# Performance work log

Measured on AMD Instinct MI355X. Metric: run time of the kernel, lower is better.

## Reference

```python
import jax, jax.numpy as jnp
import numpy as np

EPS = 1e-4
SILU_GAIN = 1.0 / 0.596  # magnitude-preserving SiLU gain
SCALES = (4, 4, 8)       # prod == A_DIM == 128
T = 0.3                  # residual lerp weight


def mp_silu(x):
    return jax.nn.silu(x) * SILU_GAIN


def pixel_norm(x):
    # normalize over channel dim (axis=1) to unit RMS
    return x * jax.lax.rsqrt(jnp.mean(jnp.square(x), axis=1, keepdims=True) + EPS)


def norm_w(w):
    # magnitude-preserving conv: per-output-filter L2-normalized weight
    n = jnp.sqrt(jnp.sum(jnp.square(w), axis=tuple(range(1, w.ndim)), keepdims=True) + 1e-8)
    return w / n


def mp_add(a, b, t=T):
    return (a * (1.0 - t) + b * t) / np.sqrt((1.0 - t) ** 2 + t ** 2)


def conv2d(x, w, groups=1, padding=((0, 0), (0, 0))):
    return jax.lax.conv_general_dilated(
        x, w, (1, 1), padding,
        dimension_numbers=('NCHW', 'OIHW', 'NCHW'), feature_group_count=groups)


def conv1d(x, w, groups=1, padding=((0, 0),)):
    return jax.lax.conv_general_dilated(
        x, w, (1,), padding,
        dimension_numbers=('NCH', 'OIH', 'NCH'), feature_group_count=groups)


def avgpool_freq(x, s):
    B, C, F, L = x.shape
    return jnp.mean(x.reshape(B, C, F // s, s, L), axis=3)


def min_gru(h, w):
    # minGRU: z_t = sigmoid(Wz h_t), c_t = Wc h_t, s_t = (1-z_t) s_{t-1} + z_t c_t
    z, c = jnp.split(conv1d(h, norm_w(w)), 2, axis=1)
    z = jax.nn.sigmoid(z)
    a, b = 1.0 - z, z * c  # linear recurrence s_t = a_t s_{t-1} + b_t

    def comb(x, y):
        a1, b1 = x
        a2, b2 = y
        return a2 * a1, a2 * b1 + b2

    _, out = jax.lax.associative_scan(comb, (a, b), axis=-1)
    return out


def conv_block(x, w1, wd, w2, wdn, s):
    # x: [B, d, F, L]
    x = pixel_norm(x)
    r = mp_silu(x)
    r = conv2d(r, norm_w(w1))                                            # d -> h, 1x1
    r = conv2d(r, norm_w(wd), groups=wd.shape[0], padding=((2, 2), (1, 1)))  # depthwise 5x3
    r = mp_silu(r)
    r = conv2d(r, norm_w(w2))                                            # h -> d, 1x1
    h = mp_add(x, r)
    return conv2d(avgpool_freq(h, s), norm_w(wdn))                       # d -> 2d, freq /s


def seq_block(x, hg_w, dw_w, gru_w, out_w):
    # x: [B, d, L]
    x = pixel_norm(x)
    h, g = jnp.split(conv1d(x, norm_w(hg_w)), 2, axis=1)  # each [B, H, L]
    h = mp_silu(h)
    h = conv1d(h, norm_w(dw_w), groups=dw_w.shape[0], padding=((1, 1),))  # depthwise k=3
    h = mp_silu(h)
    h = min_gru(h, gru_w)
    h = h * mp_silu(g)
    return mp_add(x, conv1d(h, norm_w(out_w)))


def setup_inputs() -> dict:
    key = jax.random.key(0)
    ks = jax.random.split(key, 18)
    rn = lambda k, s: jax.random.normal(k, s, dtype=jnp.float32)
    B, L, A = 2, 2048, 128
    return {
        'audio': rn(ks[0], (B, A, L)),
        'proj_w': rn(ks[1], (64, 1, 1, 1)) * 0.5,
        'proj_b': jnp.zeros((64,), jnp.float32),
        'c0_w1': rn(ks[2], (128, 64, 1, 1)),
        'c0_wd': rn(ks[3], (128, 1, 5, 3)),
        'c0_w2': rn(ks[4], (64, 128, 1, 1)),
        'c0_dn': rn(ks[5], (128, 64, 1, 1)),
        'c1_w1': rn(ks[6], (256, 128, 1, 1)),
        'c1_wd': rn(ks[7], (256, 1, 5, 3)),
        'c1_w2': rn(ks[8], (128, 256, 1, 1)),
        'c1_dn': rn(ks[9], (256, 128, 1, 1)),
        'c2_w1': rn(ks[10], (512, 256, 1, 1)),
        'c2_wd': rn(ks[11], (512, 1, 5, 3)),
        'c2_w2': rn(ks[12], (256, 512, 1, 1)),
        'c2_dn': rn(ks[13], (512, 256, 1, 1)),
        'hg_w': rn(ks[14], (4, 2048, 512, 1)),
        'dw_w': rn(ks[15], (4, 1024, 1, 3)),
        'gru_w': rn(ks[16], (4, 2048, 1024, 1)),
        'out_w': rn(ks[17], (4, 512, 1024, 1)),
    }


def reference(audio, proj_w, proj_b,
              c0_w1, c0_wd, c0_w2, c0_dn,
              c1_w1, c1_wd, c1_w2, c1_dn,
              c2_w1, c2_wd, c2_w2, c2_dn,
              hg_w, dw_w, gru_w, out_w):
    h = audio[:, None]  # [B, 1, A_DIM, L]
    h = conv2d(h, proj_w) + proj_b[None, :, None, None]
    blocks = ((c0_w1, c0_wd, c0_w2, c0_dn),
              (c1_w1, c1_wd, c1_w2, c1_dn),
              (c2_w1, c2_wd, c2_w2, c2_dn))
    for (w1, wd, w2, dn), s in zip(blocks, SCALES):
        h = conv_block(h, w1, wd, w2, dn, s)
    h = h[:, :, 0, :]  # freq dim reduced to 1 -> [B, dim, L]
    for i in range(hg_w.shape[0]):
        h = seq_block(h, hg_w[i], dw_w[i], gru_w[i], out_w[i])
    return mp_silu(h)
```

## Files before the change

kernel.cpp:

```cpp
#include <hip/hip_runtime.h>
#include <math.h>

#define GAIN 1.6778523489932886f
#define MPS  1.3130643285972254f

typedef __attribute__((ext_vector_type(8))) short short8;
typedef __attribute__((ext_vector_type(4))) short short4v;
typedef __attribute__((ext_vector_type(4))) float float4v;

__device__ __forceinline__ float silu_g(float x){
  float s = 1.0f/(1.0f + __expf(-x));
  return x*s*GAIN;
}
__device__ __forceinline__ short f2bf(float f){
  unsigned u = __builtin_bit_cast(unsigned, f);
  u += 0x7fffu + ((u >> 16) & 1u);
  return (short)(u >> 16);
}
__device__ __forceinline__ float bf2f(unsigned short h){
  return __builtin_bit_cast(float, ((unsigned)h) << 16);
}

typedef __attribute__((address_space(3))) unsigned int as3_uint;
typedef const __attribute__((address_space(1))) unsigned int as1_cuint;
__device__ __forceinline__ void gload16(const unsigned short* gsrc, unsigned short* ldst){
  __builtin_amdgcn_global_load_lds((as1_cuint*)gsrc, (as3_uint*)ldst, 16, 0, 0);
}

struct NcEnt { const float* w; int O, K, dstOff; };
struct NcArgs { NcEnt e[16]; };

__global__ __launch_bounds__(64) void normcast_kernel(NcArgs na, unsigned short* __restrict__ wbf){
  int row = blockIdx.x;
  int base = 0; int i;
  for (i = 0; i < 16; i++){
    if (row < base + na.e[i].O) break;
    base += na.e[i].O;
  }
  if (i >= 16) return;
  int r = row - base; int K = na.e[i].K;
  const float* w = na.e[i].w + (long)r*K;
  unsigned short* dst = wbf + na.e[i].dstOff + (long)r*K;
  int tid = threadIdx.x;
  float s = 0.f;
  const bool v4 = ((K & 3) == 0);
  if (v4){
    for (int k = tid*4; k < K; k += 256){
      float4v v = *(const float4v*)&w[k];
      s += v[0]*v[0] + v[1]*v[1] + v[2]*v[2] + v[3]*v[3];
    }
  } else {
    for (int k = tid; k < K; k += 64){ float v = w[k]; s += v*v; }
  }
  for (int off = 32; off; off >>= 1) s += __shfl_down(s, off);
  float inv = rsqrtf(__shfl(s, 0) + 1e-8f);
  if (v4){
    for (int k = tid*4; k < K; k += 256){
      float4v v = *(const float4v*)&w[k];
      short4v o = { f2bf(v[0]*inv), f2bf(v[1]*inv), f2bf(v[2]*inv), f2bf(v[3]*inv) };
      *(short4v*)&dst[k] = o;
    }
  } else {
    for (int k = tid; k < K; k += 64) dst[k] = (unsigned short)f2bf(w[k]*inv);
  }
}

__global__ __launch_bounds__(64) void projstats_kernel(const float* __restrict__ pw, const float* __restrict__ pb,
                                                       float* __restrict__ S){
  int t = threadIdx.x;
  float p = pw[t], q = pb[t];
  float s1 = p*p, s2 = p*q, s3 = q*q;
  for (int off = 32; off; off >>= 1){
    s1 += __shfl_down(s1, off); s2 += __shfl_down(s2, off); s3 += __shfl_down(s3, off);
  }
  if (t == 0){ S[0] = s1; S[1] = s2; S[2] = s3; }
}

__global__ __launch_bounds__(256) void invn_audio_kernel(const float* __restrict__ audio, const float* __restrict__ S,
                                                         float* __restrict__ invn){
  long i = blockIdx.x*256 + threadIdx.x;
  if (i >= (2L*128*2048)/4) return;
  long e = i*4;
  float S1 = S[0], S2 = S[1], S3 = S[2];
  float4v a = *(const float4v*)&audio[e];
  float4v o;
  #pragma unroll
  for (int j = 0; j < 4; j++) o[j] = rsqrtf((a[j]*a[j]*S1 + 2.f*a[j]*S2 + S3)/64.f + 1e-4f);
  *(float4v*)&invn[e] = o;
}

template<int G, bool BF>
__global__ __launch_bounds__(256) void invn_reduce_kernel(const void* __restrict__ Xv, float* __restrict__ invn,
                                                          int C, int F){
  constexpr int L = 256/G;
  int t = threadIdx.x; int cs = t / L; int li = t % L;
  long pos = (long)blockIdx.x*L + li;
  int bf = (int)(pos >> 11); int l = (int)(pos & 2047);
  int b = bf / F; int f = bf - b*F;
  long base = ((long)b*C*F + f)*2048 + l;
  long stride = (long)F*2048;
  float s = 0.f;
  if (BF){
    const unsigned short* X = (const unsigned short*)Xv;
    for (int c = cs; c < C; c += G){ float v = bf2f(X[base + (long)c*stride]); s += v*v; }
  } else {
    const float* X = (const float*)Xv;
    for (int c = cs; c < C; c += G){ float v = X[base + (long)c*stride]; s += v*v; }
  }
  __shared__ float red[256];
  red[t] = s; __syncthreads();
  #pragma unroll
  for (int off = G/2; off > 0; off >>= 1){
    if (cs < off) red[t] += red[t + off*L];
    __syncthreads();
  }
  if (cs == 0) invn[pos] = rsqrtf(red[li]/(float)C + 1e-4f);
}

template<bool SILU, bool BF>
__global__ __launch_bounds__(256) void applynorm_kernel(const void* __restrict__ Xv, const float* __restrict__ invn,
                                                        unsigned short* __restrict__ XB, int C, int F, long total4){
  long i = blockIdx.x*256 + threadIdx.x;
  if (i >= total4) return;
  long e = i*4;
  int l = (int)(e & 2047); long r = e >> 11;
  int f = (int)(r % F); long bc = r / F; int b = (int)(bc / C);
  float4v x;
  if (BF){
    short4v u = *(const short4v*)((const unsigned short*)Xv + e);
    x = (float4v){ bf2f((unsigned short)u[0]), bf2f((unsigned short)u[1]),
                   bf2f((unsigned short)u[2]), bf2f((unsigned short)u[3]) };
  } else {
    x = *(const float4v*)((const float*)Xv + e);
  }
  float4v iv = *(const float4v*)&invn[((long)b*F + f)*2048 + l];
  short4v o;
  #pragma unroll
  for (int j = 0; j < 4; j++){
    float v = x[j]*iv[j];
    o[j] = f2bf(SILU ? silu_g(v) : v);
  }
  *(short4v*)&XB[e] = o;
}

__global__ __launch_bounds__(256) void normT_kernel(const float* __restrict__ SEQ,
                                                    const float* __restrict__ invn,
                                                    unsigned short* __restrict__ XST){
  __shared__ float tile[64][65];
  const int l0 = blockIdx.x*64, c0 = blockIdx.y*64, b = blockIdx.z;
  const int t = threadIdx.x;
  const int lr = (t & 15)*4;
  const int cr = t >> 4;
  #pragma unroll
  for (int p = 0; p < 4; p++){
    int c = cr + p*16;
    float4v v = *(const float4v*)&SEQ[((long)(b*512 + c0 + c))*2048 + l0 + lr];
    tile[c][lr+0] = v[0]; tile[c][lr+1] = v[1]; tile[c][lr+2] = v[2]; tile[c][lr+3] = v[3];
  }
  __syncthreads();
  const int cc = (t & 7)*8;
  const int lw = t >> 3;
  #pragma unroll
  for (int p = 0; p < 2; p++){
    int l = lw + p*32;
    float iv = invn[b*2048 + l0 + l];
    short8 o;
    #pragma unroll
    for (int j = 0; j < 8; j++) o[j] = f2bf(tile[cc+j][l] * iv);
    *(short8*)&XST[((long)(b*2048 + l0 + l))*512 + c0 + cc] = o;
  }
}

struct GTArgs {
  const unsigned short* A;
  const unsigned short* B;
  unsigned short* O1;
  unsigned short* O2;
  int N, K;
};

template<int EMODE>
__global__ __launch_bounds__(256,2) void gemmT_kernel(GTArgs g){
  __shared__ __align__(16) char SMEMraw[49152];
  unsigned short (*Asm)[4096] = (unsigned short (*)[4096])SMEMraw;
  unsigned short (*Bsm)[4096] = (unsigned short (*)[4096])(SMEMraw + 24576);
  const int t = threadIdx.x;
  const int lane = t & 63;
  const int wc = (t >> 7) & 1;
  const int wsd = (t >> 6) & 1;
  const int q = lane >> 4, r16 = lane & 15;
  const int m0 = blockIdx.x * 128;
  const int n0 = blockIdx.y * 128;
  const int K = g.K;

  const int r0 = t >> 2;
  const int c8 = (((t & 3) ^ ((r0 >> 1) & 3)) << 3);
  const unsigned short* Ap = g.A + (long)(n0 + r0)*K + c8;
  const unsigned short* Bp = g.B + (long)(m0 + r0)*K + c8;

  auto stage = [&](int bi, int k0){
    gload16(Ap + k0,           &Asm[bi][t*8]);
    gload16(Ap + 64*K + k0,    &Asm[bi][2048 + t*8]);
    gload16(Bp + k0,           &Bsm[bi][t*8]);
    gload16(Bp + 64*K + k0,    &Bsm[bi][2048 + t*8]);
  };

  float4v acc[4][4];
  #pragma unroll
  for (int i = 0; i < 4; i++)
    #pragma unroll
    for (int j = 0; j < 4; j++) acc[i][j] = (float4v){0.f,0.f,0.f,0.f};

  const int nit = K >> 5;
  stage(0, 0);
  stage(1, 32);

  const int qsw = ((q ^ ((r16 >> 1) & 3)) << 3);

  for (int it = 0; it < nit; ++it){
    if (it + 2 < nit){
      stage((it + 2) % 3, (it + 2) << 5);
      asm volatile("" ::: "memory");
      asm volatile("s_waitcnt vmcnt(8)" ::: "memory");
    } else if (it + 1 < nit){
      asm volatile("s_waitcnt vmcnt(4)" ::: "memory");
    } else {
      asm volatile("s_waitcnt vmcnt(0)" ::: "memory");
    }
    __builtin_amdgcn_s_barrier();
    asm volatile("" ::: "memory");

    const unsigned short* As = Asm[it % 3];
    const unsigned short* Bs = Bsm[it % 3];
    short8 afr[4], bfr[4];
    #pragma unroll
    for (int i = 0; i < 4; i++) afr[i] = *(const short8*)&As[(wc*64 + i*16 + r16)*32 + qsw];
    #pragma unroll
    for (int j = 0; j < 4; j++) bfr[j] = *(const short8*)&Bs[(wsd*64 + j*16 + r16)*32 + qsw];
    #pragma unroll
    for (int i = 0; i < 4; i++)
      #pragma unroll
      for (int j = 0; j < 4; j++)
        acc[i][j] = __builtin_amdgcn_mfma_f32_16x16x32_bf16(afr[i], bfr[j], acc[i][j], 0, 0, 0);

    asm volatile("" ::: "memory");
    __builtin_amdgcn_s_barrier();
  }

  if (EMODE == 1 && n0 < 1024){
    float* Cf = (float*)SMEMraw;
    #pragma unroll
    for (int h = 0; h < 2; h++){
      __syncthreads();
      if (wc == h){
        #pragma unroll
        for (int j = 0; j < 4; j++){
          int m = wsd*64 + j*16 + r16;
          #pragma unroll
          for (int i = 0; i < 4; i++)
            *(float4v*)&Cf[m*68 + i*16 + q*4] = acc[i][j];
        }
      }
      __syncthreads();
      #pragma unroll
      for (int p = 0; p < 4; p++){
        int m = (t >> 3) + p*32;
        int n8 = (t & 7)*8;
        int gm = m0 + m; int b = gm >> 11, l = gm & 2047;
        float4v v0 = *(const float4v*)&Cf[m*68 + n8];
        float4v v1 = *(const float4v*)&Cf[m*68 + n8 + 4];
        short8 o;
        #pragma unroll
        for (int e = 0; e < 4; e++){ o[e] = f2bf(silu_g(v0[e])); o[e+4] = f2bf(silu_g(v1[e])); }
        *(short8*)&g.O1[((long)(b*2048 + l))*1024 + (n0 + h*64 + n8)] = o;
      }
    }
  } else {
    float* Csm = (float*)SMEMraw;
    #pragma unroll
    for (int qtr = 0; qtr < 4; qtr++){
      __syncthreads();
      if (wc == (qtr >> 1)){
        #pragma unroll
        for (int ii = 0; ii < 2; ii++){
          int i = (qtr & 1)*2 + ii;
          #pragma unroll
          for (int j = 0; j < 4; j++){
            int m = wsd*64 + j*16 + r16;
            #pragma unroll
            for (int rg = 0; rg < 4; rg++)
              Csm[(ii*16 + q*4 + rg)*132 + m] = acc[i][j][rg];
          }
        }
      }
      __syncthreads();
      #pragma unroll
      for (int sp = 0; sp < 2; sp++){
        int nrow = (t >> 4) + sp*16;
        int n = n0 + qtr*32 + nrow;
        int m8 = (t & 15)*8;
        int gm = m0 + m8; int b = gm >> 11, l = gm & 2047;
        float4v v0 = *(const float4v*)&Csm[nrow*132 + m8];
        float4v v1 = *(const float4v*)&Csm[nrow*132 + m8 + 4];
        short8 o;
        #pragma unroll
        for (int e = 0; e < 4; e++){ o[e] = f2bf(v0[e]); o[e+4] = f2bf(v1[e]); }
        if (EMODE == 1) *(short8*)&g.O2[((long)(b*1024 + (n - 1024)))*2048 + l] = o;
        else            *(short8*)&g.O1[((long)(b*2048 + n))*2048 + l] = o;
      }
    }
  }
}

struct GemmArgs {
  const unsigned short* A;
  const unsigned short* Bh;
  const float* invn; const float* audio;
  const float* pw; const float* pb;
  const unsigned short* auxXH;
  unsigned short* CoutH; unsigned short* Cout2H;
  int N, K, Fdim, Lw, lq0, BLw, Bl0, CLw, Cl0, Nsto, Fsrc;
};

template<int BMODE, int EMODE>
__global__ __launch_bounds__(256,2) void mgemm_kernel(GemmArgs g){
  __shared__ __align__(16) char SMEMraw[20480];
  unsigned short* Asm = (unsigned short*)SMEMraw;
  unsigned short* Bsm = Asm + 128*40;
  const int t = threadIdx.x;
  const int lane = t & 63;
  const int wave = t >> 6;
  const int wc = wave >> 1, wsd = wave & 1;
  const int q = lane >> 4, r16 = lane & 15;
  const int s0 = blockIdx.x * 128;
  const int n0 = blockIdx.y * 128;
  const int FL = g.Fdim * g.Lw;

  const int ar = t >> 1, ah = t & 1;
  const int an = n0 + ar;
  const bool aval = an < g.N;
  const unsigned short* Aptr = g.A + (long)an*g.K + ah*16;

  const int kg = t & 7, mg = t >> 3;
  const int mb = s0 + mg*4;
  int bcol = mb / FL; int rr = mb - bcol*FL;
  int fcol = (g.Fdim > 1) ? (rr / g.Lw) : 0;
  int labs = g.lq0 + (rr - fcol*g.Lw);
  const bool cv = (bcol < 2);
  bool lv[4];
  #pragma unroll
  for (int j = 0; j < 4; j++) lv[j] = cv && (labs + j >= 0) && (labs + j < 2048);
  const bool vec4 = cv && (labs >= 0) && (labs + 3 < 2048);
  const unsigned short* bbase = g.Bh;
  if (cv) bbase = g.Bh + ((long)(bcol*g.K)*g.Fsrc + fcol)*g.BLw + (labs - g.Bl0);
  const long kstep = (long)g.Fsrc * g.BLw;

  float invn4[4] = {0,0,0,0}, aud4[4] = {0,0,0,0};
  if (BMODE == 2){
    #pragma unroll
    for (int j = 0; j < 4; j++) if (lv[j]){
      invn4[j] = g.invn[(bcol*g.Fdim + fcol)*2048 + labs + j];
      aud4[j]  = g.audio[(bcol*128 + fcol)*2048 + labs + j];
    }
  }

  float4v acc[4][4];
  #pragma unroll
  for (int i = 0; i < 4; i++)
    #pragma unroll
    for (int j = 0; j < 4; j++) acc[i][j] = (float4v){0.f,0.f,0.f,0.f};

  short8 pa0 = {0,0,0,0,0,0,0,0}, pa1 = {0,0,0,0,0,0,0,0};
  short4v praw[4];
  #pragma unroll
  for (int i = 0; i < 4; i++) praw[i] = (short4v){0,0,0,0};

  auto ldA = [&](int kb){
    if (aval){
      pa0 = *(const short8*)(Aptr + kb);
      pa1 = *(const short8*)(Aptr + kb + 8);
    }
  };
  auto ldB = [&](int kb){
    #pragma unroll
    for (int i = 0; i < 4; i++){
      const int k = kb + kg*4 + i;
      const unsigned short* bp = bbase + (long)k*kstep;
      if (vec4) praw[i] = *(const short4v*)bp;
      else {
        short4v u = {0,0,0,0};
        #pragma unroll
        for (int j = 0; j < 4; j++) if (lv[j]) u[j] = (short)bp[j];
        praw[i] = u;
      }
    }
  };

  ldA(0);
  if (BMODE == 0) ldB(0);

  for (int k0 = 0; k0 < g.K; k0 += 32){
    short8 sa0 = pa0, sa1 = pa1;
    short4v bpk[4];
    if (BMODE == 0){
      #pragma unroll
      for (int j = 0; j < 4; j++){
        short4v p;
        #pragma unroll
        for (int i = 0; i < 4; i++) p[i] = praw[i][j];
        bpk[j] = p;
      }
    } else {
      float tv[4][4];
      #pragma unroll
      for (int i = 0; i < 4; i++){
        const int k = k0 + kg*4 + i;
        const float pwk = g.pw[k], pbk = g.pb[k];
        #pragma unroll
        for (int j = 0; j < 4; j++) tv[i][j] = lv[j] ? silu_g((aud4[j]*pwk + pbk)*invn4[j]) : 0.f;
      }
      #pragma unroll
      for (int j = 0; j < 4; j++){
        short4v p;
        #pragma unroll
        for (int i = 0; i < 4; i++) p[i] = f2bf(tv[i][j]);
        bpk[j] = p;
      }
    }
    if (k0 + 32 < g.K){
      ldA(k0 + 32);
      if (BMODE == 0) ldB(k0 + 32);
    }

    __syncthreads();
    *(short8*)&Asm[ar*40 + ah*16]     = sa0;
    *(short8*)&Asm[ar*40 + ah*16 + 8] = sa1;
    #pragma unroll
    for (int j = 0; j < 4; j++)
      *(short4v*)&Bsm[(mg*4 + j)*40 + kg*4] = bpk[j];
    __syncthreads();

    short8 afr[4], bfr[4];
    #pragma unroll
    for (int i = 0; i < 4; i++) afr[i] = *(const short8*)&Asm[(wc*64 + i*16 + r16)*40 + q*8];
    #pragma unroll
    for (int j = 0; j < 4; j++) bfr[j] = *(const short8*)&Bsm[(wsd*64 + j*16 + r16)*40 + q*8];
    #pragma unroll
    for (int i = 0; i < 4; i++)
      #pragma unroll
      for (int j = 0; j < 4; j++)
        acc[i][j] = __builtin_amdgcn_mfma_f32_16x16x32_bf16(afr[i], bfr[j], acc[i][j], 0, 0, 0);
  }

  {
    float* Csm = (float*)SMEMraw;
    #pragma unroll
    for (int qtr = 0; qtr < 4; qtr++){
      __syncthreads();
      if (wc == (qtr >> 1)){
        #pragma unroll
        for (int ii = 0; ii < 2; ii++){
          int i = (qtr & 1)*2 + ii;
          #pragma unroll
          for (int j = 0; j < 4; j++){
            int m = wsd*64 + j*16 + r16;
            #pragma unroll
            for (int rg = 0; rg < 4; rg++)
              Csm[(ii*16 + q*4 + rg)*132 + m] = acc[i][j][rg];
          }
        }
      }
      __syncthreads();
      #pragma unroll
      for (int sp = 0; sp < 2; sp++){
        int nrow = (t >> 4) + sp*16;
        int n = n0 + qtr*32 + nrow;
        int m8 = (t & 15)*8;
        if (n >= g.N) continue;
        int sg = s0 + m8;
        int b2 = sg / FL; int r2 = sg - b2*FL;
        if (b2 >= 2) continue;
        int f2 = (g.Fdim > 1) ? (r2 / g.Lw) : 0;
        int l2 = g.lq0 + (r2 - f2*g.Lw);
        float4v v0 = *(const float4v*)&Csm[nrow*132 + m8];
        float4v v1 = *(const float4v*)&Csm[nrow*132 + m8 + 4];
        long obase = ((long)(b2*g.Nsto + n)*g.Fdim + f2)*g.CLw + (l2 - g.Cl0);
        short8 o;
        if (EMODE == 1){
          #pragma unroll
          for (int e = 0; e < 4; e++){ o[e] = f2bf(v0[e]); o[e+4] = f2bf(v1[e]); }
        } else if (EMODE == 2){
          short8 axv = *(const short8*)&g.auxXH[((long)(b2*g.N + n)*g.Fdim + f2)*2048 + l2];
          const float* ivp = &g.invn[(b2*g.Fdim + f2)*2048 + l2];
          float4v iv0 = *(const float4v*)ivp;
          float4v iv1 = *(const float4v*)(ivp + 4);
          #pragma unroll
          for (int e = 0; e < 4; e++){
            float xn0 = bf2f((unsigned short)axv[e]) * iv0[e];
            float xn1 = bf2f((unsigned short)axv[e+4]) * iv1[e];
            o[e]   = f2bf((xn0*0.7f + v0[e]*0.3f)*MPS);
            o[e+4] = f2bf((xn1*0.7f + v1[e]*0.3f)*MPS);
          }
        } else {
          float pwn = g.pw[n], pbn = g.pb[n];
          const float* ap  = &g.audio[(b2*128 + f2)*2048 + l2];
          const float* ivp = &g.invn[(b2*g.Fdim + f2)*2048 + l2];
          float4v a0 = *(const float4v*)ap,  a1 = *(const float4v*)(ap + 4);
          float4v iv0 = *(const float4v*)ivp, iv1 = *(const float4v*)(ivp + 4);
          #pragma unroll
          for (int e = 0; e < 4; e++){
            float xn0 = (a0[e]*pwn + pbn)*iv0[e];
            float xn1 = (a1[e]*pwn + pbn)*iv1[e];
            o[e]   = f2bf((xn0*0.7f + v0[e]*0.3f)*MPS);
            o[e+4] = f2bf((xn1*0.7f + v1[e]*0.3f)*MPS);
          }
        }
        *(short8*)&g.CoutH[obase] = o;
      }
    }
  }
}

struct DnArgs {
  const unsigned short* A; const unsigned short* P;
  float* Cout; unsigned short* CoutH;
  int N, K, F2, Lc, l0;
};

template<int EMODE>
__global__ __launch_bounds__(256,4) void mgemm64_kernel(DnArgs g){
  __shared__ __align__(16) unsigned short Asm[64*40];
  __shared__ __align__(16) unsigned short Bsm[64*40];
  const int t = threadIdx.x;
  const int lane = t & 63;
  const int wave = t >> 6;
  const int wc = wave >> 1, wsd = wave & 1;
  const int q = lane >> 4, r16 = lane & 15;
  const int s0 = blockIdx.x * 64;
  const int n0 = blockIdx.y * 64;
  const int FL = g.F2 * g.Lc;

  const int ar = t >> 2, ah = t & 3;
  const unsigned short* Aptr = g.A + (long)(n0 + ar)*g.K + ah*8;
  const int kg = t & 7, mg = t >> 3;
  const bool bstage = (mg < 16);
  const int mb = s0 + (mg & 15)*4;
  const int bcol = mb / FL; const int rr = mb - bcol*FL;
  const int fcol = rr / g.Lc; const int li = rr - fcol*g.Lc;
  const unsigned short* bbase = g.P + ((long)(bcol*g.K)*g.F2 + fcol)*g.Lc + li;
  const long kstep = (long)g.F2 * g.Lc;

  float4v acc[2][2];
  #pragma unroll
  for (int i = 0; i < 2; i++)
    #pragma unroll
    for (int j = 0; j < 2; j++) acc[i][j] = (float4v){0.f,0.f,0.f,0.f};

  short8 pa = {0,0,0,0,0,0,0,0};
  short4v praw[4];
  #pragma unroll
  for (int i = 0; i < 4; i++) praw[i] = (short4v){0,0,0,0};

  auto ldA = [&](int kb){ pa = *(const short8*)(Aptr + kb); };
  auto ldB = [&](int kb){
    if (bstage){
      #pragma unroll
      for (int i = 0; i < 4; i++)
        praw[i] = *(const short4v*)(bbase + (long)(kb + kg*4 + i)*kstep);
    }
  };
  ldA(0); ldB(0);

  for (int k0 = 0; k0 < g.K; k0 += 32){
    short8 sa = pa;
    short4v bpk[4];
    #pragma unroll
    for (int j = 0; j < 4; j++){
      short4v p;
      #pragma unroll
      for (int i = 0; i < 4; i++) p[i] = praw[i][j];
      bpk[j] = p;
    }
    if (k0 + 32 < g.K){ ldA(k0 + 32); ldB(k0 + 32); }

    __syncthreads();
    *(short8*)&Asm[ar*40 + ah*8] = sa;
    if (bstage){
      #pragma unroll
      for (int j = 0; j < 4; j++)
        *(short4v*)&Bsm[((mg & 15)*4 + j)*40 + kg*4] = bpk[j];
    }
    __syncthreads();

    short8 afr[2], bfr[2];
    #pragma unroll
    for (int i = 0; i < 2; i++) afr[i] = *(const short8*)&Asm[(wc*32 + i*16 + r16)*40 + q*8];
    #pragma unroll
    for (int j = 0; j < 2; j++) bfr[j] = *(const short8*)&Bsm[(wsd*32 + j*16 + r16)*40 + q*8];
    #pragma unroll
    for (int i = 0; i < 2; i++)
      #pragma unroll
      for (int j = 0; j < 2; j++)
        acc[i][j] = __builtin_amdgcn_mfma_f32_16x16x32_bf16(afr[i], bfr[j], acc[i][j], 0, 0, 0);
  }

  #pragma unroll
  for (int j = 0; j < 2; j++){
    int sg = s0 + wsd*32 + j*16 + r16;
    int b2 = sg / FL; int r2 = sg - b2*FL;
    int f2 = r2 / g.Lc; int l2 = g.l0 + (r2 - f2*g.Lc);
    #pragma unroll
    for (int i = 0; i < 2; i++){
      #pragma unroll
      for (int rg = 0; rg < 4; rg++){
        int n = n0 + wc*32 + i*16 + q*4 + rg;
        float v = acc[i][j][rg];
        long oidx = ((long)(b2*g.N + n)*g.F2 + f2)*2048 + l2;
        if (EMODE == 0) g.Cout[oidx] = v;
        else            g.CoutH[oidx] = (unsigned short)f2bf(v);
      }
    }
  }
}

template<int EMODE>
__global__ __launch_bounds__(256,4) void seqout_kernel(const unsigned short* __restrict__ A,
                                                       const unsigned short* __restrict__ Bh,
                                                       const float* __restrict__ invn,
                                                       const float* __restrict__ auxX,
                                                       float* __restrict__ Cout, int K){
  __shared__ __align__(16) unsigned short Asm[64*40];
  __shared__ __align__(16) unsigned short Bsm[64*40];
  const int t = threadIdx.x;
  const int lane = t & 63;
  const int wave = t >> 6;
  const int wc = wave >> 1, wsd = wave & 1;
  const int q = lane >> 4, r16 = lane & 15;
  const int s0 = blockIdx.x * 64;
  const int n0 = blockIdx.y * 64;

  const int ar = t >> 2, ah = t & 3;
  const unsigned short* Aptr = A + (long)(n0 + ar)*K + ah*8;
  const int kg = t & 7, mg = t >> 3;
  const bool bstage = (mg < 16);
  const int mb = s0 + (mg & 15)*4;
  const int bcol = mb >> 11, lb = mb & 2047;
  const unsigned short* bbase = Bh + ((long)bcol*K)*2048 + lb;

  float4v acc[2][2];
  #pragma unroll
  for (int i = 0; i < 2; i++)
    #pragma unroll
    for (int j = 0; j < 2; j++) acc[i][j] = (float4v){0.f,0.f,0.f,0.f};

  short8 pa = {0,0,0,0,0,0,0,0};
  short4v praw[4];
  #pragma unroll
  for (int i = 0; i < 4; i++) praw[i] = (short4v){0,0,0,0};

  auto ldA = [&](int kb){ pa = *(const short8*)(Aptr + kb); };
  auto ldB = [&](int kb){
    if (bstage){
      #pragma unroll
      for (int i = 0; i < 4; i++)
        praw[i] = *(const short4v*)(bbase + (long)(kb + kg*4 + i)*2048);
    }
  };
  ldA(0); ldB(0);

  for (int k0 = 0; k0 < K; k0 += 32){
    short8 sa = pa;
    short4v bpk[4];
    #pragma unroll
    for (int j = 0; j < 4; j++){
      short4v p;
      #pragma unroll
      for (int i = 0; i < 4; i++) p[i] = praw[i][j];
      bpk[j] = p;
    }
    if (k0 + 32 < K){ ldA(k0 + 32); ldB(k0 + 32); }

    __syncthreads();
    *(short8*)&Asm[ar*40 + ah*8] = sa;
    if (bstage){
      #pragma unroll
      for (int j = 0; j < 4; j++)
        *(short4v*)&Bsm[((mg & 15)*4 + j)*40 + kg*4] = bpk[j];
    }
    __syncthreads();

    short8 afr[2], bfr[2];
    #pragma unroll
    for (int i = 0; i < 2; i++) afr[i] = *(const short8*)&Asm[(wc*32 + i*16 + r16)*40 + q*8];
    #pragma unroll
    for (int j = 0; j < 2; j++) bfr[j] = *(const short8*)&Bsm[(wsd*32 + j*16 + r16)*40 + q*8];
    #pragma unroll
    for (int i = 0; i < 2; i++)
      #pragma unroll
      for (int j = 0; j < 2; j++)
        acc[i][j] = __builtin_amdgcn_mfma_f32_16x16x32_bf16(afr[i], bfr[j], acc[i][j], 0, 0, 0);
  }

  #pragma unroll
  for (int j = 0; j < 2; j++){
    int sg = s0 + wsd*32 + j*16 + r16;
    int b2 = sg >> 11, l2 = sg & 2047;
    float invn_p = invn[b2*2048 + l2];
    #pragma unroll
    for (int i = 0; i < 2; i++){
      #pragma unroll
      for (int rg = 0; rg < 4; rg++){
        int n = n0 + wc*32 + i*16 + q*4 + rg;
        float v = acc[i][j][rg];
        float xn = auxX[((long)b2*512 + n)*2048 + l2] * invn_p;
        float r = (xn*0.7f + v*0.3f)*MPS;
        if (EMODE == 6) r = silu_g(r);
        Cout[((long)b2*512 + n)*2048 + l2] = r;
      }
    }
  }
}

__global__ __launch_bounds__(256) void poolf_kernel(const unsigned short* __restrict__ Hb,
                                                    unsigned short* __restrict__ P,
                                                    int F2, int s, int Lc, long total4){
  long i = blockIdx.x*256 + threadIdx.x;
  if (i >= total4) return;
  long e = i*4;
  int li = (int)(e % Lc); long r0 = e / Lc;
  int f2 = (int)(r0 % F2); long r = r0 / F2;
  const unsigned short* src = Hb + ((long)r*F2*s + (long)f2*s)*Lc + li;
  float a0=0,a1=0,a2=0,a3=0;
  for (int p = 0; p < s; p++){
    short4v u = *(const short4v*)(src + (long)p*Lc);
    a0 += bf2f((unsigned short)u[0]); a1 += bf2f((unsigned short)u[1]);
    a2 += bf2f((unsigned short)u[2]); a3 += bf2f((unsigned short)u[3]);
  }
  float inv = 1.f/(float)s;
  short4v o = { f2bf(a0*inv), f2bf(a1*inv), f2bf(a2*inv), f2bf(a3*inv) };
  *(short4v*)&P[((long)r*F2 + f2)*Lc + li] = o;
}

struct DwArgs { const unsigned short* R1; const unsigned short* wd; unsigned short* R2; int C, F, Lc, l0; };
__global__ __launch_bounds__(256) void dw2d_kernel(DwArgs a){
  int idx = blockIdx.x*256 + threadIdx.x;
  int Lq = a.Lc >> 3;
  int Fq = a.F >> 2;
  int total = 2*a.C*Fq*Lq;
  if (idx >= total) return;
  int lq = idx % Lq; int r = idx / Lq;
  int fq = r % Fq; r /= Fq;
  int c = r % a.C; int b = r / a.C;
  int f0 = fq*4;
  int labs = a.l0 + lq*8;
  int Lw = a.Lc + 8;
  const unsigned short* base = a.R1 + (long)((b*a.C + c)*a.F)*Lw + (labs - (a.l0 - 4));
  const unsigned short* w = a.wd + c*15;
  float W[5][3];
  #pragma unroll
  for (int tp = 0; tp < 5; tp++)
    #pragma unroll
    for (int j = 0; j < 3; j++) W[tp][j] = bf2f(w[tp*3 + j]);

  const bool llo = (labs > 0);
  const bool lhi = (labs + 8 < 2048);
  float acc[4][8];
  #pragma unroll
  for (int t = 0; t < 4; t++)
    #pragma unroll
    for (int j = 0; j < 8; j++) acc[t][j] = 0.f;

  #pragma unroll
  for (int r8 = 0; r8 < 8; r8++){
    int rrow = f0 - 2 + r8;
    if (rrow < 0 || rrow >= a.F) continue;
    const unsigned short* p = base + (long)rrow*Lw;
    short4v u0 = *(const short4v*)p;
    short4v u1 = *(const short4v*)(p + 4);
    float x[10];
    x[0] = llo ? bf2f(p[-1]) : 0.f;
    x[1] = bf2f((unsigned short)u0[0]); x[2] = bf2f((unsigned short)u0[1]);
    x[3] = bf2f((unsigned short)u0[2]); x[4] = bf2f((unsigned short)u0[3]);
    x[5] = bf2f((unsigned short)u1[0]); x[6] = bf2f((unsigned short)u1[1]);
    x[7] = bf2f((unsigned short)u1[2]); x[8] = bf2f((unsigned short)u1[3]);
    x[9] = lhi ? bf2f(p[8]) : 0.f;
    #pragma unroll
    for (int t = 0; t < 4; t++){
      const int df = r8 - 2 - t;
      if (df < -2 || df > 2) continue;
      float w0 = W[df+2][0], w1 = W[df+2][1], w2 = W[df+2][2];
      #pragma unroll
      for (int j = 0; j < 8; j++)
        acc[t][j] += w0*x[j] + w1*x[j+1] + w2*x[j+2];
    }
  }

  unsigned short* ob = a.R2 + ((long)((b*a.C + c)*a.F + f0))*a.Lc + (labs - a.l0);
  #pragma unroll
  for (int t = 0; t < 4; t++){
    short8 o;
    #pragma unroll
    for (int j = 0; j < 8; j++) o[j] = f2bf(silu_g(acc[t][j]));
    *(short8*)(ob + (long)t*a.Lc) = o;
  }
}

__global__ __launch_bounds__(256) void dwseqT_kernel(const unsigned short* __restrict__ HST,
                                                     const unsigned short* __restrict__ w,
                                                     unsigned short* __restrict__ H2T){
  int idx = blockIdx.x*256 + threadIdx.x;
  if (idx >= 2*2048*128) return;
  int c0 = (idx & 127) * 8; long bt = idx >> 7;
  int tt = (int)(bt & 2047);
  const unsigned short* base = HST + bt*1024 + c0;
  short8 zz = {0,0,0,0,0,0,0,0};
  short8 x1 = *(const short8*)base;
  short8 x0 = (tt > 0)    ? *(const short8*)(base - 1024) : zz;
  short8 x2 = (tt < 2047) ? *(const short8*)(base + 1024) : zz;
  const unsigned short* wp = w + c0*3;
  short8 o;
  #pragma unroll
  for (int j = 0; j < 8; j++){
    float w0 = bf2f(wp[3*j]), w1 = bf2f(wp[3*j+1]), w2 = bf2f(wp[3*j+2]);
    float v = w0*bf2f((unsigned short)x0[j]) + w1*bf2f((unsigned short)x1[j]) + w2*bf2f((unsigned short)x2[j]);
    o[j] = f2bf(silu_g(v));
  }
  *(short8*)&H2T[bt*1024 + c0] = o;
}

__global__ __launch_bounds__(256) void scan_kernel(const unsigned short* __restrict__ ZC, const unsigned short* __restrict__ G,
                                                   unsigned short* __restrict__ SC){
  int bc = blockIdx.x;
  int b = bc >> 10, c = bc & 1023;
  const unsigned short* zrow = ZC + ((long)(b*2048 + c))*2048;
  const unsigned short* crow = ZC + ((long)(b*2048 + 1024 + c))*2048;
  const unsigned short* grow = G + (long)bc*2048;
  unsigned short* orow = SC + (long)bc*2048;
  int tid = threadIdx.x;
  int t0 = tid*8;
  short8 zv = *(const short8*)&zrow[t0];
  short8 cv = *(const short8*)&crow[t0];
  float av[8], bv[8];
  float A = 1.f, Bv = 0.f;
  #pragma unroll
  for (int j = 0; j < 8; j++){
    float z = bf2f((unsigned short)zv[j]); float cval = bf2f((unsigned short)cv[j]);
    float zs = 1.f/(1.f + __expf(-z));
    float a = 1.f - zs; float bb = zs*cval;
    av[j] = a; bv[j] = bb;
    Bv = a*Bv + bb;
    A = a*A;
  }
  __shared__ float sA[256], sB[256];
  sA[tid] = A; sB[tid] = Bv;
  __syncthreads();
  for (int off = 1; off < 256; off <<= 1){
    float pA = 1.f, pB = 0.f;
    if (tid >= off){ pA = sA[tid-off]; pB = sB[tid-off]; }
    __syncthreads();
    float nA = A*pA; float nB = A*pB + Bv;
    A = nA; Bv = nB;
    sA[tid] = A; sB[tid] = Bv;
    __syncthreads();
  }
  float h = (tid > 0) ? sB[tid-1] : 0.f;
  short8 gv = *(const short8*)&grow[t0];
  short8 ov;
  #pragma unroll
  for (int j = 0; j < 8; j++){
    h = av[j]*h + bv[j];
    ov[j] = f2bf(h * silu_g(bf2f((unsigned short)gv[j])));
  }
  *(short8*)&orow[t0] = ov;
}

extern "C" void kernel_launch(void* const* d_in, const int* in_sizes, int n_in,
                              void* d_out, int out_size, void* d_ws, size_t ws_size,
                              hipStream_t stream) {
  const float* audio = (const float*)d_in[0];
  const float* pw = (const float*)d_in[1];
  const float* pb = (const float*)d_in[2];
  const float* cw1[3] = {(const float*)d_in[3], (const float*)d_in[7], (const float*)d_in[11]};
  const float* cwd[3] = {(const float*)d_in[4], (const float*)d_in[8], (const float*)d_in[12]};
  const float* cw2[3] = {(const float*)d_in[5], (const float*)d_in[9], (const float*)d_in[13]};
  const float* cdn[3] = {(const float*)d_in[6], (const float*)d_in[10], (const float*)d_in[14]};
  const float* hgw  = (const float*)d_in[15];
  const float* dww  = (const float*)d_in[16];
  const float* gruw = (const float*)d_in[17];
  const float* outw = (const float*)d_in[18];
  float* out = (float*)d_out;

  char* P0 = (char*)d_ws;
  float*          INVW = (float*)P0;                    P0 += 131072;
  unsigned short* WBF  = (unsigned short*)P0;           P0 += 30443776;
  float*          INVN = (float*)P0;                    P0 += 2097152;
  char*           XBZC = P0;                            P0 += 33554432;
  unsigned short* IN1h = (unsigned short*)P0;           P0 += 33554432;
  unsigned short* IN2h = (unsigned short*)P0;           P0 += 16777216;
  float*          SEQ  = (float*)P0;                    P0 += 8388608;
  char*           ARENA = P0;
  long arenaBytes = (long)ws_size - (long)(P0 - (char*)d_ws);
  float* S = INVW + 32000;

  const float* wsrc[16] = {cw1[0],cwd[0],cw2[0],cdn[0], cw1[1],cwd[1],cw2[1],cdn[1],
                           cw1[2],cwd[2],cw2[2],cdn[2], hgw, dww, gruw, outw};
  int Os[16] = {128,128,64,128, 256,256,128,256, 512,512,256,512, 8192,4096,8192,2048};
  int Ks[16] = {64,15,128,64, 128,15,256,128, 256,15,512,256, 512,3,1024,1024};
  int wbfOff[16];
  {
    int wo = 0;
    for (int i = 0; i < 16; i++){ wbfOff[i] = wo; wo += Os[i]*Ks[i]; }
  }
  {
    NcArgs na;
    int rows = 0;
    for (int i = 0; i < 16; i++){
      na.e[i].w = wsrc[i]; na.e[i].O = Os[i]; na.e[i].K = Ks[i]; na.e[i].dstOff = wbfOff[i];
      rows += Os[i];
    }
    normcast_kernel<<<rows, 64, 0, stream>>>(na, WBF);
  }
  projstats_kernel<<<1, 64, 0, stream>>>(pw, pb, S);

  int Cin_[3]  = {64,128,256};
  int Cmid_[3] = {128,256,512};
  int F_[3]    = {128,32,8};
  int s_[3]    = {4,4,8};
  const unsigned short* XinH[3] = {nullptr, IN1h, IN2h};
  unsigned short* XoutH[3] = {IN1h, IN2h, nullptr};
  int iW1[3]={0,4,8}, iWd[3]={1,5,9}, iW2[3]={2,6,10}, iDn[3]={3,7,11};

  for (int b = 0; b < 3; b++){
    int Cin = Cin_[b], Cmid = Cmid_[b], F = F_[b], s = s_[b];
    int F2 = F/s;
    int nc = 16;
    for (int c = 1; c <= 16; c <<= 1){
      long Lc = 2048/c;
      long bytes = 2L*(2L*Cmid*F*(Lc+8) + 2L*Cmid*F*Lc + 2L*Cin*F*Lc + 2L*Cin*F2*Lc);
      if (bytes <= arenaBytes){ nc = c; break; }
    }
    int Lc = 2048/nc;
    unsigned short* R1 = (unsigned short*)ARENA;
    unsigned short* R2 = R1 + 2L*Cmid*F*(Lc+8);
    unsigned short* Hb = R2 + 2L*Cmid*F*Lc;
    unsigned short* Pb = Hb + 2L*Cin*F*Lc;
    unsigned short* XB = (unsigned short*)XBZC;

    if (b == 0){
      invn_audio_kernel<<<(2*128*2048/4+255)/256, 256, 0, stream>>>(audio, S, INVN);
    } else {
      int positions = 2*F*2048;
      invn_reduce_kernel<8,true><<<positions/32, 256, 0, stream>>>(XinH[b], INVN, Cin, F);
      long total4 = (long)2*Cin*F*2048/4;
      applynorm_kernel<true,true><<<(int)((total4+255)/256), 256, 0, stream>>>(XinH[b], INVN, XB, Cin, F, total4);
    }

    for (int ci = 0; ci < nc; ci++){
      int l0 = ci*Lc;
      GemmArgs ga{};
      ga.A = WBF + wbfOff[iW1[b]];
      ga.Bh = XB; ga.invn = INVN; ga.audio = audio; ga.pw = pw; ga.pb = pb;
      ga.CoutH = R1; ga.N = Cmid; ga.K = Cin; ga.Fdim = F; ga.Lw = Lc+8; ga.lq0 = l0-4;
      ga.BLw = 2048; ga.Bl0 = 0; ga.CLw = Lc+8; ga.Cl0 = l0-4; ga.Nsto = Cmid; ga.Fsrc = F;
      int M1 = 2*F*(Lc+8);
      dim3 g1((M1+127)/128, (Cmid+127)/128);
      if (b == 0) mgemm_kernel<2,1><<<g1,256,0,stream>>>(ga);
      else        mgemm_kernel<0,1><<<g1,256,0,stream>>>(ga);
      DwArgs da{R1, WBF + wbfOff[iWd[b]], R2, Cmid, F, Lc, l0};
      int tdw = 2*Cmid*(F/4)*(Lc/8);
      dw2d_kernel<<<(tdw+255)/256, 256, 0, stream>>>(da);
      GemmArgs gb{};
      gb.A = WBF + wbfOff[iW2[b]];
      gb.Bh = R2; gb.invn = INVN; gb.audio = audio; gb.pw = pw; gb.pb = pb; gb.auxXH = XinH[b];
      gb.CoutH = Hb; gb.N = Cin; gb.K = Cmid; gb.Fdim = F; gb.Lw = Lc; gb.lq0 = l0;
      gb.BLw = Lc; gb.Bl0 = l0; gb.CLw = Lc; gb.Cl0 = l0; gb.Nsto = Cin; gb.Fsrc = F;
      int M2 = 2*F*Lc;
      dim3 g2((M2+127)/128, (Cin+127)/128);
      if (b == 0) mgemm_kernel<0,3><<<g2,256,0,stream>>>(gb);
      else        mgemm_kernel<0,2><<<g2,256,0,stream>>>(gb);
      long tp4 = (2L*Cin*F2*Lc)/4;
      poolf_kernel<<<(int)((tp4+255)/256), 256, 0, stream>>>(Hb, Pb, F2, s, Lc, tp4);
      DnArgs dn{};
      dn.A = WBF + wbfOff[iDn[b]]; dn.P = Pb;
      dn.Cout = SEQ; dn.CoutH = XoutH[b];
      dn.N = Cmid; dn.K = Cin; dn.F2 = F2; dn.Lc = Lc; dn.l0 = l0;
      dim3 gdn((2*F2*Lc)/64, Cmid/64);
      if (b == 2) mgemm64_kernel<0><<<gdn,256,0,stream>>>(dn);
      else        mgemm64_kernel<1><<<gdn,256,0,stream>>>(dn);
    }
  }

  unsigned short* XST = IN1h;
  unsigned short* HST = XST + 2097152;
  unsigned short* G   = HST + 4194304;
  unsigned short* H2T = G  + 4194304;
  unsigned short* SC  = H2T + 4194304;
  unsigned short* ZCh = (unsigned short*)XBZC;

  for (int i = 0; i < 4; i++){
    invn_reduce_kernel<16,false><<<4096/16, 256, 0, stream>>>(SEQ, INVN, 512, 1);
    normT_kernel<<<dim3(32,8,2), 256, 0, stream>>>(SEQ, INVN, XST);
    GTArgs gh{ WBF + wbfOff[12] + (long)i*2048*512, XST, HST, G, 2048, 512 };
    gemmT_kernel<1><<<dim3(32,16), 256, 0, stream>>>(gh);
    dwseqT_kernel<<<2048, 256, 0, stream>>>(HST, WBF + wbfOff[13] + i*1024*3, H2T);
    GTArgs gz{ WBF + wbfOff[14] + (long)i*2048*1024, H2T, ZCh, nullptr, 2048, 1024 };
    gemmT_kernel<0><<<dim3(32,16), 256, 0, stream>>>(gz);
    scan_kernel<<<2048,256,0,stream>>>(ZCh, G, SC);
    const unsigned short* oA = WBF + wbfOff[15] + (long)i*512*1024;
    if (i < 3) seqout_kernel<5><<<dim3(64,8),256,0,stream>>>(oA, SC, INVN, SEQ, SEQ, 1024);
    else       seqout_kernel<6><<<dim3(64,8),256,0,stream>>>(oA, SC, INVN, SEQ, out, 1024);
  }

  (void)in_sizes; (void)n_in; (void)out_size;
}
```

Measured before the change: 1.106 ms.

## Fuse pixel-norm and SiLU into GEMM B-load; stage GEMM epilogues through LDS

Drops the separate applynorm pass for conv blocks 1 and 2. The first 1x1 GEMM gains a new B mode that loads the raw bf16 input and applies the inverse norm and SiLU gain while packing tiles, which saves a full write and read of the normalized activation. Separately, the 64-wide GEMM epilogues now stage accumulators through shared memory so each thread writes coalesced float4/short4 rows instead of scattered scalar stores. This adds extra barriers and recomputes the SiLU for every N-tile that reads the same B data.

```diff
diff --git a/kernel.cpp b/kernel.cpp
--- a/kernel.cpp
+++ b/kernel.cpp
@@ -117,32 +117,6 @@
   if (cs == 0) invn[pos] = rsqrtf(red[li]/(float)C + 1e-4f);
 }
 
-template<bool SILU, bool BF>
-__global__ __launch_bounds__(256) void applynorm_kernel(const void* __restrict__ Xv, const float* __restrict__ invn,
-                                                        unsigned short* __restrict__ XB, int C, int F, long total4){
-  long i = blockIdx.x*256 + threadIdx.x;
-  if (i >= total4) return;
-  long e = i*4;
-  int l = (int)(e & 2047); long r = e >> 11;
-  int f = (int)(r % F); long bc = r / F; int b = (int)(bc / C);
-  float4v x;
-  if (BF){
-    short4v u = *(const short4v*)((const unsigned short*)Xv + e);
-    x = (float4v){ bf2f((unsigned short)u[0]), bf2f((unsigned short)u[1]),
-                   bf2f((unsigned short)u[2]), bf2f((unsigned short)u[3]) };
-  } else {
-    x = *(const float4v*)((const float*)Xv + e);
-  }
-  float4v iv = *(const float4v*)&invn[((long)b*F + f)*2048 + l];
-  short4v o;
-  #pragma unroll
-  for (int j = 0; j < 4; j++){
-    float v = x[j]*iv[j];
-    o[j] = f2bf(SILU ? silu_g(v) : v);
-  }
-  *(short4v*)&XB[e] = o;
-}
-
 __global__ __launch_bounds__(256) void normT_kernel(const float* __restrict__ SEQ,
                                                     const float* __restrict__ invn,
                                                     unsigned short* __restrict__ XST){
@@ -356,11 +330,11 @@
   const long kstep = (long)g.Fsrc * g.BLw;
 
   float invn4[4] = {0,0,0,0}, aud4[4] = {0,0,0,0};
-  if (BMODE == 2){
+  if (BMODE == 2 || BMODE == 3){
     #pragma unroll
     for (int j = 0; j < 4; j++) if (lv[j]){
       invn4[j] = g.invn[(bcol*g.Fdim + fcol)*2048 + labs + j];
-      aud4[j]  = g.audio[(bcol*128 + fcol)*2048 + labs + j];
+      if (BMODE == 2) aud4[j] = g.audio[(bcol*128 + fcol)*2048 + labs + j];
     }
   }
 
@@ -397,7 +371,7 @@
   };
 
   ldA(0);
-  if (BMODE == 0) ldB(0);
+  if (BMODE != 2) ldB(0);
 
   for (int k0 = 0; k0 < g.K; k0 += 32){
     short8 sa0 = pa0, sa1 = pa1;
@@ -410,6 +384,15 @@
         for (int i = 0; i < 4; i++) p[i] = praw[i][j];
         bpk[j] = p;
       }
+    } else if (BMODE == 3){
+      #pragma unroll
+      for (int j = 0; j < 4; j++){
+        short4v p;
+        #pragma unroll
+        for (int i = 0; i < 4; i++)
+          p[i] = f2bf(silu_g(bf2f((unsigned short)praw[i][j]) * invn4[j]));
+        bpk[j] = p;
+      }
     } else {
       float tv[4][4];
       #pragma unroll
@@ -429,7 +412,7 @@
     }
     if (k0 + 32 < g.K){
       ldA(k0 + 32);
-      if (BMODE == 0) ldB(k0 + 32);
+      if (BMODE != 2) ldB(k0 + 32);
     }
 
     __syncthreads();
@@ -529,8 +512,9 @@
 
 template<int EMODE>
 __global__ __launch_bounds__(256,4) void mgemm64_kernel(DnArgs g){
-  __shared__ __align__(16) unsigned short Asm[64*40];
-  __shared__ __align__(16) unsigned short Bsm[64*40];
+  __shared__ __align__(16) char SMEM[10240];
+  unsigned short* Asm = (unsigned short*)SMEM;
+  unsigned short* Bsm = Asm + 64*40;
   const int t = threadIdx.x;
   const int lane = t & 63;
   const int wave = t >> 6;
@@ -604,20 +588,32 @@
         acc[i][j] = __builtin_amdgcn_mfma_f32_16x16x32_bf16(afr[i], bfr[j], acc[i][j], 0, 0, 0);
   }
 
-  #pragma unroll
-  for (int j = 0; j < 2; j++){
-    int sg = s0 + wsd*32 + j*16 + r16;
-    int b2 = sg / FL; int r2 = sg - b2*FL;
-    int f2 = r2 / g.Lc; int l2 = g.l0 + (r2 - f2*g.Lc);
-    #pragma unroll
-    for (int i = 0; i < 2; i++){
-      #pragma unroll
-      for (int rg = 0; rg < 4; rg++){
-        int n = n0 + wc*32 + i*16 + q*4 + rg;
-        float v = acc[i][j][rg];
-        long oidx = ((long)(b2*g.N + n)*g.F2 + f2)*2048 + l2;
-        if (EMODE == 0) g.Cout[oidx] = v;
-        else            g.CoutH[oidx] = (unsigned short)f2bf(v);
+  {
+    float* Csm = (float*)SMEM;
+    const int b2 = s0 / FL; const int r20 = s0 - b2*FL;
+    const int f2c = r20 / g.Lc; const int l2c = g.l0 + (r20 - f2c*g.Lc);
+    #pragma unroll
+    for (int nq = 0; nq < 4; nq++){
+      __syncthreads();
+      if (wc == (nq >> 1)){
+        const int i = nq & 1;
+        #pragma unroll
+        for (int j = 0; j < 2; j++)
+          #pragma unroll
+          for (int rg = 0; rg < 4; rg++)
+            Csm[(q*4 + rg)*68 + wsd*32 + j*16 + r16] = acc[i][j][rg];
+      }
+      __syncthreads();
+      int nrow = t >> 4;
+      int mq = (t & 15)*4;
+      int n = n0 + nq*16 + nrow;
+      float4v v = *(const float4v*)&Csm[nrow*68 + mq];
+      long oidx = ((long)(b2*g.N + n)*g.F2 + f2c)*2048 + l2c + mq;
+      if (EMODE == 0){
+        *(float4v*)&g.Cout[oidx] = v;
+      } else {
+        short4v o = { f2bf(v[0]), f2bf(v[1]), f2bf(v[2]), f2bf(v[3]) };
+        *(short4v*)&g.CoutH[oidx] = o;
       }
     }
   }
@@ -629,8 +625,9 @@
                                                        const float* __restrict__ invn,
                                                        const float* __restrict__ auxX,
                                                        float* __restrict__ Cout, int K){
-  __shared__ __align__(16) unsigned short Asm[64*40];
-  __shared__ __align__(16) unsigned short Bsm[64*40];
+  __shared__ __align__(16) char SMEM[10240];
+  unsigned short* Asm = (unsigned short*)SMEM;
+  unsigned short* Bsm = Asm + 64*40;
   const int t = threadIdx.x;
   const int lane = t & 63;
   const int wave = t >> 6;
@@ -701,22 +698,36 @@
         acc[i][j] = __builtin_amdgcn_mfma_f32_16x16x32_bf16(afr[i], bfr[j], acc[i][j], 0, 0, 0);
   }
 
-  #pragma unroll
-  for (int j = 0; j < 2; j++){
-    int sg = s0 + wsd*32 + j*16 + r16;
-    int b2 = sg >> 11, l2 = sg & 2047;
-    float invn_p = invn[b2*2048 + l2];
-    #pragma unroll
-    for (int i = 0; i < 2; i++){
-      #pragma unroll
-      for (int rg = 0; rg < 4; rg++){
-        int n = n0 + wc*32 + i*16 + q*4 + rg;
-        float v = acc[i][j][rg];
-        float xn = auxX[((long)b2*512 + n)*2048 + l2] * invn_p;
-        float r = (xn*0.7f + v*0.3f)*MPS;
-        if (EMODE == 6) r = silu_g(r);
-        Cout[((long)b2*512 + n)*2048 + l2] = r;
-      }
+  {
+    float* Csm = (float*)SMEM;
+    const int b2 = s0 >> 11; const int l0b = s0 & 2047;
+    #pragma unroll
+    for (int nq = 0; nq < 4; nq++){
+      __syncthreads();
+      if (wc == (nq >> 1)){
+        const int i = nq & 1;
+        #pragma unroll
+        for (int j = 0; j < 2; j++)
+          #pragma unroll
+          for (int rg = 0; rg < 4; rg++)
+            Csm[(q*4 + rg)*68 + wsd*32 + j*16 + r16] = acc[i][j][rg];
+      }
+      __syncthreads();
+      int nrow = t >> 4;
+      int mq = (t & 15)*4;
+      int n = n0 + nq*16 + nrow;
+      int l = l0b + mq;
+      float4v v = *(const float4v*)&Csm[nrow*68 + mq];
+      float4v ax = *(const float4v*)&auxX[((long)b2*512 + n)*2048 + l];
+      float4v iv = *(const float4v*)&invn[b2*2048 + l];
+      float4v r;
+      #pragma unroll
+      for (int e = 0; e < 4; e++){
+        float xn = ax[e]*iv[e];
+        float rr = (xn*0.7f + v[e]*0.3f)*MPS;
+        r[e] = (EMODE == 6) ? silu_g(rr) : rr;
+      }
+      *(float4v*)&Cout[((long)b2*512 + n)*2048 + l] = r;
     }
   }
 }
@@ -944,28 +955,25 @@
     unsigned short* R2 = R1 + 2L*Cmid*F*(Lc+8);
     unsigned short* Hb = R2 + 2L*Cmid*F*Lc;
     unsigned short* Pb = Hb + 2L*Cin*F*Lc;
-    unsigned short* XB = (unsigned short*)XBZC;
 
     if (b == 0){
       invn_audio_kernel<<<(2*128*2048/4+255)/256, 256, 0, stream>>>(audio, S, INVN);
     } else {
       int positions = 2*F*2048;
       invn_reduce_kernel<8,true><<<positions/32, 256, 0, stream>>>(XinH[b], INVN, Cin, F);
-      long total4 = (long)2*Cin*F*2048/4;
-      applynorm_kernel<true,true><<<(int)((total4+255)/256), 256, 0, stream>>>(XinH[b], INVN, XB, Cin, F, total4);
     }
 
     for (int ci = 0; ci < nc; ci++){
       int l0 = ci*Lc;
       GemmArgs ga{};
       ga.A = WBF + wbfOff[iW1[b]];
-      ga.Bh = XB; ga.invn = INVN; ga.audio = audio; ga.pw = pw; ga.pb = pb;
+      ga.Bh = XinH[b]; ga.invn = INVN; ga.audio = audio; ga.pw = pw; ga.pb = pb;
       ga.CoutH = R1; ga.N = Cmid; ga.K = Cin; ga.Fdim = F; ga.Lw = Lc+8; ga.lq0 = l0-4;
       ga.BLw = 2048; ga.Bl0 = 0; ga.CLw = Lc+8; ga.Cl0 = l0-4; ga.Nsto = Cmid; ga.Fsrc = F;
       int M1 = 2*F*(Lc+8);
       dim3 g1((M1+127)/128, (Cmid+127)/128);
       if (b == 0) mgemm_kernel<2,1><<<g1,256,0,stream>>>(ga);
-      else        mgemm_kernel<0,1><<<g1,256,0,stream>>>(ga);
+      else        mgemm_kernel<3,1><<<g1,256,0,stream>>>(ga);
       DwArgs da{R1, WBF + wbfOff[iWd[b]], R2, Cmid, F, Lc, l0};
       int tdw = 2*Cmid*(F/4)*(Lc/8);
       dw2d_kernel<<<(tdw+255)/256, 256, 0, stream>>>(da);
```

After: 1.108 ms. No clear change (+0.2%).
